# Optimization experiments

Hardware: AMD Instinct MI355X
Metric: run time of the kernel (lower is better)

The kernel has to match this reference:

```python
import jax, jax.numpy as jnp
import numpy as np

VOCAB, HIDDEN, BATCH, T = 32000, 256, 16, 256


def setup_inputs() -> dict:
    key = jax.random.key(0)
    ks = jax.random.split(key, 8)
    s_in = 1.0 / np.sqrt(HIDDEN)  # torch nn.RNN init scale (1/sqrt(hidden))
    inputs = jax.random.randint(ks[0], (BATCH, T), 0, VOCAB)
    targets = jax.random.randint(ks[1], (BATCH, T), 0, VOCAB)
    # RNN params: torch stores W_ih as (hidden, vocab); we keep the transpose
    # (vocab, hidden) so one_hot(x) @ W_ih.T == Wih[x] (an exact gather).
    Wih = jax.random.uniform(ks[2], (VOCAB, HIDDEN), minval=-s_in, maxval=s_in)
    bih = jax.random.uniform(ks[3], (HIDDEN,), minval=-s_in, maxval=s_in)
    Whh = jax.random.uniform(ks[4], (HIDDEN, HIDDEN), minval=-s_in, maxval=s_in)
    bhh = jax.random.uniform(ks[5], (HIDDEN,), minval=-s_in, maxval=s_in)
    Wfc = jax.random.uniform(ks[6], (VOCAB, HIDDEN), minval=-s_in, maxval=s_in)
    bfc = jax.random.uniform(ks[7], (VOCAB,), minval=-s_in, maxval=s_in)
    return {"inputs": inputs, "targets": targets, "Wih": Wih, "bih": bih,
            "Whh": Whh, "bhh": bhh, "Wfc": Wfc, "bfc": bfc}


def reference(inputs, targets, Wih, bih, Whh, bhh, Wfc, bfc):
    # one_hot(inputs) @ W_ih.T + b_ih  ==  Wih[inputs] + bih (exact same math)
    xproj = Wih[inputs] + bih                      # (B, T, H)
    B = inputs.shape[0]
    h0 = jnp.zeros((B, HIDDEN), dtype=Wih.dtype)

    def step(h, xt):
        h = jnp.tanh(xt + h @ Whh.T + bhh)
        return h, h

    _, hs = jax.lax.scan(step, h0, jnp.swapaxes(xproj, 0, 1))  # (T, B, H)
    hs = jnp.swapaxes(hs, 0, 1)                    # (B, T, H)
    logits = hs @ Wfc.T + bfc                      # (B, T, V)
    logp = jax.nn.log_softmax(logits, axis=-1)
    nll = -jnp.take_along_axis(logp, targets[..., None], axis=-1)
    return jnp.mean(nll)                           # scalar cross-entropy loss
```

## Files before the change

### kernel.cpp

```cpp
#include <hip/hip_runtime.h>
#include <hip/hip_bf16.h>
#include <stdint.h>

#define VOCAB 32000
#define HID   256
#define BATCH 16
#define SEQT  256
#define ROWS  (BATCH*SEQT)

typedef __attribute__((ext_vector_type(8))) short bf16x8_t;
typedef __attribute__((ext_vector_type(4))) float f32x4_t;

__device__ __forceinline__ short f2bs(float x) {
    __hip_bfloat16 h = __float2bfloat16(x);
    return *reinterpret_cast<short*>(&h);
}
__device__ __forceinline__ bf16x8_t cvt8(float4 a, float4 b) {
    union { short s[8]; bf16x8_t v; } u;
    u.s[0] = f2bs(a.x); u.s[1] = f2bs(a.y); u.s[2] = f2bs(a.z); u.s[3] = f2bs(a.w);
    u.s[4] = f2bs(b.x); u.s[5] = f2bs(b.y); u.s[6] = f2bs(b.z); u.s[7] = f2bs(b.w);
    return u.v;
}
__device__ __forceinline__ void barrier_lds() {
    asm volatile("s_waitcnt lgkmcnt(0)\n\ts_barrier" ::: "memory");
}
__device__ __forceinline__ float tanh_cf(float x) {
    float x2 = x * x;
    float nm = x * fmaf(x2, x2 + 105.f, 945.f);
    float dn = fmaf(x2, fmaf(x2, 15.f, 420.f), 945.f);
    float h = nm * __builtin_amdgcn_rcpf(dn);
    return fminf(fmaxf(h, -1.f), 1.f);
}
__device__ __forceinline__ short rne_bf16(float x) {
    uint32_t u = __float_as_uint(x);
    uint32_t r = (u + 0x7FFFu + ((u >> 16) & 1u)) >> 16;
    return (short)r;
}

__global__ __launch_bounds__(256) void xproj_kernel(
    const int* __restrict__ inputs,
    const float* __restrict__ Wih,
    const float* __restrict__ bih,
    const float* __restrict__ bhh,
    const float* __restrict__ Wfc,
    float* __restrict__ xp,
    float* __restrict__ S,
    __hip_bfloat16* __restrict__ Wfcb,
    int do_cvt)
{
    int idx = blockIdx.x * 256 + threadIdx.x;
    int h  = idx & 255;
    int tb = idx >> 8;
    int b  = tb & 15;
    int t  = tb >> 4;
    int id = inputs[b * SEQT + t];
    xp[idx] = Wih[(size_t)id * HID + h] + bih[h] + bhh[h];
    if (idx < ROWS) S[idx] = 0.0f;
    if (do_cvt && idx < (VOCAB * HID / 8)) {
        const float4* p = (const float4*)(Wfc + (size_t)idx * 8);
        *(bf16x8_t*)((short*)Wfcb + (size_t)idx * 8) = cvt8(p[0], p[1]);
    }
}

__global__ __launch_bounds__(512, 1) void rnn_kernel(
    const float* __restrict__ xp,
    const float* __restrict__ Whh,
    __hip_bfloat16* __restrict__ hs)
{
    __shared__ short hbuf[2][16][264];
    const int tid = threadIdx.x;
    const int l = tid & 63, w = tid >> 6;
    const int lr = l & 15, lh = l >> 4;
    const int cm = tid >> 5;
    const int cc = (tid & 31) * 8;

    bf16x8_t bfrag[2][8];
#pragma unroll
    for (int nt = 0; nt < 2; nt++) {
        int n = w * 32 + nt * 16 + lr;
#pragma unroll
        for (int ki = 0; ki < 8; ki++) {
            const float4* p = (const float4*)(Whh + n * HID + ki * 32 + lh * 8);
            bfrag[nt][ki] = cvt8(p[0], p[1]);
        }
    }
    for (int i = tid; i < 16 * 264; i += 512) ((short*)hbuf[0])[i] = 0;
    __syncthreads();

    float xv[2][4];
#pragma unroll
    for (int nt = 0; nt < 2; nt++) {
        int n = w * 32 + nt * 16 + lr;
#pragma unroll
        for (int r = 0; r < 4; r++)
            xv[nt][r] = xp[(lh * 4 + r) * HID + n];
    }

    int cur = 0;
    for (int t = 0; t < SEQT; t++) {
        if (t > 0) {
            bf16x8_t hv = *(const bf16x8_t*)(&hbuf[cur][cm][cc]);
            *(bf16x8_t*)((short*)hs + (size_t)(t - 1) * BATCH * HID + cm * HID + cc) = hv;
        }

        bf16x8_t afr[8];
#pragma unroll
        for (int ki = 0; ki < 8; ki++)
            afr[ki] = *(const bf16x8_t*)(&hbuf[cur][lr][ki * 32 + lh * 8]);

        f32x4_t a0a = {0,0,0,0}, a0b = {0,0,0,0}, a1a = {0,0,0,0}, a1b = {0,0,0,0};
#pragma unroll
        for (int ki = 0; ki < 4; ki++) {
            a0a = __builtin_amdgcn_mfma_f32_16x16x32_bf16(afr[ki],     bfrag[0][ki],     a0a, 0, 0, 0);
            a0b = __builtin_amdgcn_mfma_f32_16x16x32_bf16(afr[ki + 4], bfrag[0][ki + 4], a0b, 0, 0, 0);
            a1a = __builtin_amdgcn_mfma_f32_16x16x32_bf16(afr[ki],     bfrag[1][ki],     a1a, 0, 0, 0);
            a1b = __builtin_amdgcn_mfma_f32_16x16x32_bf16(afr[ki + 4], bfrag[1][ki + 4], a1b, 0, 0, 0);
        }

        float xn[2][4] = {{0,0,0,0},{0,0,0,0}};
        if (t + 1 < SEQT) {
            const float* xbase = xp + (size_t)(t + 1) * BATCH * HID;
#pragma unroll
            for (int nt = 0; nt < 2; nt++) {
                int n = w * 32 + nt * 16 + lr;
#pragma unroll
                for (int r = 0; r < 4; r++)
                    xn[nt][r] = xbase[(lh * 4 + r) * HID + n];
            }
        }

#pragma unroll
        for (int nt = 0; nt < 2; nt++) {
            int n = w * 32 + nt * 16 + lr;
#pragma unroll
            for (int r = 0; r < 4; r++) {
                float v = (nt ? (a1a[r] + a1b[r]) : (a0a[r] + a0b[r])) + xv[nt][r];
                hbuf[cur ^ 1][lh * 4 + r][n] = rne_bf16(tanh_cf(v));
            }
        }
#pragma unroll
        for (int nt = 0; nt < 2; nt++)
#pragma unroll
            for (int r = 0; r < 4; r++) xv[nt][r] = xn[nt][r];
        cur ^= 1;
        barrier_lds();
    }
    bf16x8_t hv = *(const bf16x8_t*)(&hbuf[cur][cm][cc]);
    *(bf16x8_t*)((short*)hs + (size_t)(SEQT - 1) * BATCH * HID + cm * HID + cc) = hv;
}

template <bool BF16B>
__global__ __launch_bounds__(256) void fc_kernel(
    const __hip_bfloat16* __restrict__ hs,
    const void* __restrict__ WfcP,
    const float* __restrict__ bfc,
    const int* __restrict__ targets,
    float* __restrict__ S,
    float* __restrict__ TL)
{
    __shared__ short As[2][4 * 128 * 8];
    __shared__ short Bs[2][4 * 128 * 8];
    __shared__ int tgt[128];

    const int bid = blockIdx.x;
    const int xcd = bid & 7;
    const int j   = bid >> 3;
    const int m_id = j & 31;
    const int n_id = (j >> 5) * 8 + xcd;
    if (n_id >= VOCAB / 128) return;
    const int m0 = m_id * 128, n0 = n_id * 128;

    const int tid = threadIdx.x;
    const int l = tid & 63, w = tid >> 6;
    const int lr = l & 15, lh = l >> 4;
    const int wm = (w >> 1) * 64, wn = (w & 1) * 64;
    const int row = tid & 127, sub = tid >> 7;

    if (tid < 128) {
        int r = m0 + tid;
        tgt[tid] = targets[((r & 15) << 8) | (r >> 4)];
    }

    f32x4_t acc[4][4];
    const f32x4_t z = {0.f, 0.f, 0.f, 0.f};
#pragma unroll
    for (int i = 0; i < 4; i++)
#pragma unroll
        for (int jj = 0; jj < 4; jj++) acc[i][jj] = z;

    const __hip_bfloat16* gA = hs + (size_t)(m0 + row) * HID + sub * 8;
    const __hip_bfloat16* gBb = (const __hip_bfloat16*)WfcP + (size_t)(n0 + row) * HID + sub * 8;
    const float*          gBf = (const float*)WfcP + (size_t)(n0 + row) * HID + sub * 8;

    bf16x8_t rA0, rA1, rB0, rB1;
    float4 rf0a, rf0b, rf1a, rf1b;

    {
        rA0 = *(const bf16x8_t*)(gA);
        rA1 = *(const bf16x8_t*)(gA + 16);
        *(bf16x8_t*)&As[0][(sub * 128 + row) * 8] = rA0;
        *(bf16x8_t*)&As[0][((sub + 2) * 128 + row) * 8] = rA1;
        if (BF16B) {
            rB0 = *(const bf16x8_t*)(gBb);
            rB1 = *(const bf16x8_t*)(gBb + 16);
            *(bf16x8_t*)&Bs[0][(sub * 128 + row) * 8] = rB0;
            *(bf16x8_t*)&Bs[0][((sub + 2) * 128 + row) * 8] = rB1;
        } else {
            const float4* p0 = (const float4*)(gBf);
            const float4* p1 = (const float4*)(gBf + 16);
            *(bf16x8_t*)&Bs[0][(sub * 128 + row) * 8] = cvt8(p0[0], p0[1]);
            *(bf16x8_t*)&Bs[0][((sub + 2) * 128 + row) * 8] = cvt8(p1[0], p1[1]);
        }
    }
    {
        rA0 = *(const bf16x8_t*)(gA + 32);
        rA1 = *(const bf16x8_t*)(gA + 48);
        if (BF16B) {
            rB0 = *(const bf16x8_t*)(gBb + 32);
            rB1 = *(const bf16x8_t*)(gBb + 48);
        } else {
            rf0a = ((const float4*)(gBf + 32))[0]; rf0b = ((const float4*)(gBf + 32))[1];
            rf1a = ((const float4*)(gBf + 48))[0]; rf1b = ((const float4*)(gBf + 48))[1];
        }
    }
    __syncthreads();

    for (int s = 0; s < 8; s++) {
        const int buf = s & 1;
        bf16x8_t a[4], b[4];
#pragma unroll
        for (int mt = 0; mt < 4; mt++)
            a[mt] = *(const bf16x8_t*)&As[buf][(lh * 128 + wm + mt * 16 + lr) * 8];
#pragma unroll
        for (int nt = 0; nt < 4; nt++)
            b[nt] = *(const bf16x8_t*)&Bs[buf][(lh * 128 + wn + nt * 16 + lr) * 8];

        if (s + 1 < 8) {
            *(bf16x8_t*)&As[buf ^ 1][(sub * 128 + row) * 8] = rA0;
            *(bf16x8_t*)&As[buf ^ 1][((sub + 2) * 128 + row) * 8] = rA1;
            if (BF16B) {
                *(bf16x8_t*)&Bs[buf ^ 1][(sub * 128 + row) * 8] = rB0;
                *(bf16x8_t*)&Bs[buf ^ 1][((sub + 2) * 128 + row) * 8] = rB1;
            } else {
                *(bf16x8_t*)&Bs[buf ^ 1][(sub * 128 + row) * 8] = cvt8(rf0a, rf0b);
                *(bf16x8_t*)&Bs[buf ^ 1][((sub + 2) * 128 + row) * 8] = cvt8(rf1a, rf1b);
            }
        }
        if (s + 2 < 8) {
            int k0 = (s + 2) * 32;
            rA0 = *(const bf16x8_t*)(gA + k0);
            rA1 = *(const bf16x8_t*)(gA + k0 + 16);
            if (BF16B) {
                rB0 = *(const bf16x8_t*)(gBb + k0);
                rB1 = *(const bf16x8_t*)(gBb + k0 + 16);
            } else {
                rf0a = ((const float4*)(gBf + k0))[0];      rf0b = ((const float4*)(gBf + k0))[1];
                rf1a = ((const float4*)(gBf + k0 + 16))[0]; rf1b = ((const float4*)(gBf + k0 + 16))[1];
            }
        }
#pragma unroll
        for (int mt = 0; mt < 4; mt++)
#pragma unroll
            for (int nt = 0; nt < 4; nt++)
                acc[mt][nt] = __builtin_amdgcn_mfma_f32_16x16x32_bf16(a[mt], b[nt], acc[mt][nt], 0, 0, 0);
        barrier_lds();
    }

    int tg[16];
#pragma unroll
    for (int i = 0; i < 16; i++)
        tg[i] = tgt[wm + (i >> 2) * 16 + lh * 4 + (i & 3)];

    float rsum[16];
#pragma unroll
    for (int i = 0; i < 16; i++) rsum[i] = 0.f;
#pragma unroll
    for (int nt = 0; nt < 4; nt++) {
        int n = n0 + wn + nt * 16 + lr;
        float bias = bfc[n];
#pragma unroll
        for (int mt = 0; mt < 4; mt++)
#pragma unroll
            for (int r = 0; r < 4; r++) {
                float v = acc[mt][nt][r] + bias;
                rsum[mt * 4 + r] += __expf(v);
                if (tg[mt * 4 + r] == n)
                    TL[m0 + wm + mt * 16 + lh * 4 + r] = v;
            }
    }
#pragma unroll
    for (int m = 1; m < 16; m <<= 1)
#pragma unroll
        for (int i = 0; i < 16; i++) rsum[i] += __shfl_xor(rsum[i], m, 64);
    if (lr == 0) {
#pragma unroll
        for (int i = 0; i < 16; i++) {
            int r = m0 + wm + (i >> 2) * 16 + lh * 4 + (i & 3);
            atomicAdd(&S[r], rsum[i]);
        }
    }
}

__global__ __launch_bounds__(256) void loss_kernel(
    const float* __restrict__ S,
    const float* __restrict__ TL,
    float* __restrict__ out)
{
    int tid = threadIdx.x;
    float p = 0.f;
    for (int i = tid; i < ROWS; i += 256) p += __logf(S[i]) - TL[i];
#pragma unroll
    for (int m = 1; m < 64; m <<= 1) p += __shfl_xor(p, m, 64);
    __shared__ float red[4];
    if ((tid & 63) == 0) red[tid >> 6] = p;
    __syncthreads();
    if (tid == 0)
        out[0] = (red[0] + red[1] + red[2] + red[3]) / (float)ROWS;
}

extern "C" void kernel_launch(void* const* d_in, const int* in_sizes, int n_in,
                              void* d_out, int out_size, void* d_ws, size_t ws_size,
                              hipStream_t stream)
{
    (void)in_sizes; (void)n_in; (void)out_size;
    const int*   inputs  = (const int*)d_in[0];
    const int*   targets = (const int*)d_in[1];
    const float* Wih = (const float*)d_in[2];
    const float* bih = (const float*)d_in[3];
    const float* Whh = (const float*)d_in[4];
    const float* bhh = (const float*)d_in[5];
    const float* Wfc = (const float*)d_in[6];
    const float* bfc = (const float*)d_in[7];

    float* S  = (float*)d_ws;
    float* TL = S + ROWS;
    float* xp = TL + ROWS;
    __hip_bfloat16* hs = (__hip_bfloat16*)(xp + (size_t)SEQT * BATCH * HID);
    __hip_bfloat16* Wfcb = hs + (size_t)ROWS * HID;

    const size_t need = (size_t)(2 * ROWS) * 4 + (size_t)ROWS * HID * 4
                      + (size_t)ROWS * HID * 2 + (size_t)VOCAB * HID * 2;
    const int use_bf16b = (ws_size >= need) ? 1 : 0;

    xproj_kernel<<<(SEQT * BATCH * HID) / 256, 256, 0, stream>>>(
        inputs, Wih, bih, bhh, Wfc, xp, S, Wfcb, use_bf16b);
    rnn_kernel<<<1, 512, 0, stream>>>(xp, Whh, hs);
    if (use_bf16b)
        fc_kernel<true><<<8192, 256, 0, stream>>>(hs, (const void*)Wfcb, bfc, targets, S, TL);
    else
        fc_kernel<false><<<8192, 256, 0, stream>>>(hs, (const void*)Wfc, bfc, targets, S, TL);
    loss_kernel<<<1, 256, 0, stream>>>(S, TL, (float*)d_out);
}
```

Baseline: 451.1 us.

## Fuse RNN recurrence with FC/softmax tiles via atomic-flag producer-consumer overlap

Merges the single-block RNN kernel and the FC/log-sum-exp kernel into one launch. The first block to arrive runs the recurrence and publishes progress every 8 timesteps through a global atomic counter. The remaining blocks take 256x128 output tiles and spin-wait until the hidden-state rows they need exist. This lets the large vocabulary GEMM overlap the serial recurrence instead of waiting for it to finish. It also transposes the xproj layout so each lane reads a float4, seeds the MFMA accumulators with the input projection, and enlarges the M tile to 256 with 512 threads. The cost is a deadlock risk if the recurrence block is not resident, plus spin-wait overhead and a different tile shape.

```diff
diff --git a/kernel.cpp b/kernel.cpp
--- a/kernel.cpp
+++ b/kernel.cpp
@@ -7,6 +7,9 @@
 #define BATCH 16
 #define SEQT  256
 #define ROWS  (BATCH*SEQT)
+#define NPAN  (VOCAB/128)
+#define MTILES (ROWS/256)
+#define NTILES (MTILES*NPAN)
 
 typedef __attribute__((ext_vector_type(8))) short bf16x8_t;
 typedef __attribute__((ext_vector_type(4))) float f32x4_t;
@@ -45,218 +48,203 @@
     const float* __restrict__ Wfc,
     float* __restrict__ xp,
     float* __restrict__ S,
+    unsigned* __restrict__ ctrl,
     __hip_bfloat16* __restrict__ Wfcb,
     int do_cvt)
 {
-    int idx = blockIdx.x * 256 + threadIdx.x;
-    int h  = idx & 255;
-    int tb = idx >> 8;
-    int b  = tb & 15;
-    int t  = tb >> 4;
-    int id = inputs[b * SEQT + t];
-    xp[idx] = Wih[(size_t)id * HID + h] + bih[h] + bhh[h];
-    if (idx < ROWS) S[idx] = 0.0f;
+    const int tid = threadIdx.x, blk = blockIdx.x;
+    const int t = blk >> 4, hb = (blk & 15) << 4;
+    const int b = tid & 15, h = hb + (tid >> 4);
+    const int id = inputs[b * SEQT + t];
+    xp[(t * HID + h) * BATCH + b] = Wih[(size_t)id * HID + h] + bih[h] + bhh[h];
+    const int idx = blk * 256 + tid;
+    if (idx < ROWS) S[idx] = 0.f;
+    if (idx < 2) ctrl[idx] = 0u;
     if (do_cvt && idx < (VOCAB * HID / 8)) {
         const float4* p = (const float4*)(Wfc + (size_t)idx * 8);
         *(bf16x8_t*)((short*)Wfcb + (size_t)idx * 8) = cvt8(p[0], p[1]);
     }
 }
 
-__global__ __launch_bounds__(512, 1) void rnn_kernel(
+template <bool BF16B>
+__global__ __launch_bounds__(512) void fused_kernel(
     const float* __restrict__ xp,
     const float* __restrict__ Whh,
-    __hip_bfloat16* __restrict__ hs)
-{
-    __shared__ short hbuf[2][16][264];
-    const int tid = threadIdx.x;
-    const int l = tid & 63, w = tid >> 6;
-    const int lr = l & 15, lh = l >> 4;
-    const int cm = tid >> 5;
-    const int cc = (tid & 31) * 8;
-
-    bf16x8_t bfrag[2][8];
-#pragma unroll
-    for (int nt = 0; nt < 2; nt++) {
-        int n = w * 32 + nt * 16 + lr;
-#pragma unroll
-        for (int ki = 0; ki < 8; ki++) {
-            const float4* p = (const float4*)(Whh + n * HID + ki * 32 + lh * 8);
-            bfrag[nt][ki] = cvt8(p[0], p[1]);
-        }
-    }
-    for (int i = tid; i < 16 * 264; i += 512) ((short*)hbuf[0])[i] = 0;
-    __syncthreads();
-
-    float xv[2][4];
-#pragma unroll
-    for (int nt = 0; nt < 2; nt++) {
-        int n = w * 32 + nt * 16 + lr;
-#pragma unroll
-        for (int r = 0; r < 4; r++)
-            xv[nt][r] = xp[(lh * 4 + r) * HID + n];
-    }
-
-    int cur = 0;
-    for (int t = 0; t < SEQT; t++) {
-        if (t > 0) {
-            bf16x8_t hv = *(const bf16x8_t*)(&hbuf[cur][cm][cc]);
-            *(bf16x8_t*)((short*)hs + (size_t)(t - 1) * BATCH * HID + cm * HID + cc) = hv;
-        }
-
-        bf16x8_t afr[8];
-#pragma unroll
-        for (int ki = 0; ki < 8; ki++)
-            afr[ki] = *(const bf16x8_t*)(&hbuf[cur][lr][ki * 32 + lh * 8]);
-
-        f32x4_t a0a = {0,0,0,0}, a0b = {0,0,0,0}, a1a = {0,0,0,0}, a1b = {0,0,0,0};
-#pragma unroll
-        for (int ki = 0; ki < 4; ki++) {
-            a0a = __builtin_amdgcn_mfma_f32_16x16x32_bf16(afr[ki],     bfrag[0][ki],     a0a, 0, 0, 0);
-            a0b = __builtin_amdgcn_mfma_f32_16x16x32_bf16(afr[ki + 4], bfrag[0][ki + 4], a0b, 0, 0, 0);
-            a1a = __builtin_amdgcn_mfma_f32_16x16x32_bf16(afr[ki],     bfrag[1][ki],     a1a, 0, 0, 0);
-            a1b = __builtin_amdgcn_mfma_f32_16x16x32_bf16(afr[ki + 4], bfrag[1][ki + 4], a1b, 0, 0, 0);
-        }
-
-        float xn[2][4] = {{0,0,0,0},{0,0,0,0}};
-        if (t + 1 < SEQT) {
-            const float* xbase = xp + (size_t)(t + 1) * BATCH * HID;
-#pragma unroll
-            for (int nt = 0; nt < 2; nt++) {
-                int n = w * 32 + nt * 16 + lr;
-#pragma unroll
-                for (int r = 0; r < 4; r++)
-                    xn[nt][r] = xbase[(lh * 4 + r) * HID + n];
-            }
-        }
-
-#pragma unroll
-        for (int nt = 0; nt < 2; nt++) {
-            int n = w * 32 + nt * 16 + lr;
-#pragma unroll
-            for (int r = 0; r < 4; r++) {
-                float v = (nt ? (a1a[r] + a1b[r]) : (a0a[r] + a0b[r])) + xv[nt][r];
-                hbuf[cur ^ 1][lh * 4 + r][n] = rne_bf16(tanh_cf(v));
-            }
-        }
-#pragma unroll
-        for (int nt = 0; nt < 2; nt++)
-#pragma unroll
-            for (int r = 0; r < 4; r++) xv[nt][r] = xn[nt][r];
-        cur ^= 1;
-        barrier_lds();
-    }
-    bf16x8_t hv = *(const bf16x8_t*)(&hbuf[cur][cm][cc]);
-    *(bf16x8_t*)((short*)hs + (size_t)(SEQT - 1) * BATCH * HID + cm * HID + cc) = hv;
-}
-
-template <bool BF16B>
-__global__ __launch_bounds__(256) void fc_kernel(
-    const __hip_bfloat16* __restrict__ hs,
+    __hip_bfloat16* __restrict__ hs,
     const void* __restrict__ WfcP,
     const float* __restrict__ bfc,
     const int* __restrict__ targets,
     float* __restrict__ S,
-    float* __restrict__ TL)
+    float* __restrict__ TL,
+    unsigned* __restrict__ ctrl)
 {
-    __shared__ short As[2][4 * 128 * 8];
+    __shared__ short As[2][4 * 256 * 8];
     __shared__ short Bs[2][4 * 128 * 8];
-    __shared__ int tgt[128];
-
-    const int bid = blockIdx.x;
-    const int xcd = bid & 7;
-    const int j   = bid >> 3;
-    const int m_id = j & 31;
-    const int n_id = (j >> 5) * 8 + xcd;
-    if (n_id >= VOCAB / 128) return;
-    const int m0 = m_id * 128, n0 = n_id * 128;
+    __shared__ short hbuf[2][16][264];
+    __shared__ int   tgt[256];
+    __shared__ unsigned role;
 
     const int tid = threadIdx.x;
+    if (tid == 0) role = atomicAdd(&ctrl[0], 1u);
+    __syncthreads();
+    const unsigned my_role = role;
+
     const int l = tid & 63, w = tid >> 6;
     const int lr = l & 15, lh = l >> 4;
-    const int wm = (w >> 1) * 64, wn = (w & 1) * 64;
-    const int row = tid & 127, sub = tid >> 7;
-
-    if (tid < 128) {
+
+    if (my_role == 0) {
+        const int cm = tid >> 5;
+        const int cc = (tid & 31) * 8;
+        const int n0_ = w * 32 + lr, n1_ = n0_ + 16;
+
+        bf16x8_t bfrag[2][8];
+#pragma unroll
+        for (int nt = 0; nt < 2; nt++) {
+            int n = nt ? n1_ : n0_;
+#pragma unroll
+            for (int ki = 0; ki < 8; ki++) {
+                const float4* p = (const float4*)(Whh + n * HID + ki * 32 + lh * 8);
+                bfrag[nt][ki] = cvt8(p[0], p[1]);
+            }
+        }
+        for (int i = tid; i < 16 * 264; i += 512) ((short*)hbuf[0])[i] = 0;
+        __syncthreads();
+
+        float4 xv0 = *(const float4*)(xp + (size_t)n0_ * BATCH + lh * 4);
+        float4 xv1 = *(const float4*)(xp + (size_t)n1_ * BATCH + lh * 4);
+
+        int cur = 0;
+        for (int t = 0; t < SEQT; t++) {
+            if (t > 0) {
+                bf16x8_t hv = *(const bf16x8_t*)(&hbuf[cur][cm][cc]);
+                *(bf16x8_t*)((short*)hs + (size_t)(t - 1) * BATCH * HID + cm * HID + cc) = hv;
+                if ((t & 7) == 0) {
+                    asm volatile("s_waitcnt vmcnt(0)" ::: "memory");
+                    __syncthreads();
+                    if (tid == 0)
+                        __hip_atomic_store(&ctrl[1], (unsigned)t, __ATOMIC_RELEASE,
+                                           __HIP_MEMORY_SCOPE_AGENT);
+                }
+            }
+
+            bf16x8_t afr[8];
+#pragma unroll
+            for (int ki = 0; ki < 8; ki++)
+                afr[ki] = *(const bf16x8_t*)(&hbuf[cur][lr][ki * 32 + lh * 8]);
+
+            f32x4_t a0a = {xv0.x, xv0.y, xv0.z, xv0.w}, a0b = {0, 0, 0, 0};
+            f32x4_t a1a = {xv1.x, xv1.y, xv1.z, xv1.w}, a1b = {0, 0, 0, 0};
+#pragma unroll
+            for (int ki = 0; ki < 4; ki++) {
+                a0a = __builtin_amdgcn_mfma_f32_16x16x32_bf16(afr[ki],     bfrag[0][ki],     a0a, 0, 0, 0);
+                a0b = __builtin_amdgcn_mfma_f32_16x16x32_bf16(afr[ki + 4], bfrag[0][ki + 4], a0b, 0, 0, 0);
+                a1a = __builtin_amdgcn_mfma_f32_16x16x32_bf16(afr[ki],     bfrag[1][ki],     a1a, 0, 0, 0);
+                a1b = __builtin_amdgcn_mfma_f32_16x16x32_bf16(afr[ki + 4], bfrag[1][ki + 4], a1b, 0, 0, 0);
+            }
+
+            float4 xn0 = {0,0,0,0}, xn1 = {0,0,0,0};
+            if (t + 1 < SEQT) {
+                const float* xb = xp + (size_t)(t + 1) * HID * BATCH + lh * 4;
+                xn0 = *(const float4*)(xb + (size_t)n0_ * BATCH);
+                xn1 = *(const float4*)(xb + (size_t)n1_ * BATCH);
+            }
+
+#pragma unroll
+            for (int r = 0; r < 4; r++) {
+                hbuf[cur ^ 1][lh * 4 + r][n0_] = rne_bf16(tanh_cf(a0a[r] + a0b[r]));
+                hbuf[cur ^ 1][lh * 4 + r][n1_] = rne_bf16(tanh_cf(a1a[r] + a1b[r]));
+            }
+            xv0 = xn0; xv1 = xn1;
+            cur ^= 1;
+            barrier_lds();
+        }
+        {
+            bf16x8_t hv = *(const bf16x8_t*)(&hbuf[cur][cm][cc]);
+            *(bf16x8_t*)((short*)hs + (size_t)(SEQT - 1) * BATCH * HID + cm * HID + cc) = hv;
+            asm volatile("s_waitcnt vmcnt(0)" ::: "memory");
+            __syncthreads();
+            if (tid == 0)
+                __hip_atomic_store(&ctrl[1], (unsigned)SEQT, __ATOMIC_RELEASE,
+                                   __HIP_MEMORY_SCOPE_AGENT);
+        }
+        return;
+    }
+
+    const unsigned tile = my_role - 1;
+    if (tile >= NTILES) return;
+    const int mt_ = tile / NPAN, nt_ = tile % NPAN;
+    const int m0 = mt_ * 256, n0g = nt_ * 128;
+
+    if (tid < 256) {
         int r = m0 + tid;
         tgt[tid] = targets[((r & 15) << 8) | (r >> 4)];
     }
+    if (tid == 0) {
+        const unsigned need = (unsigned)((mt_ + 1) * 16);
+        while (atomicAdd(&ctrl[1], 0u) < need)
+            __builtin_amdgcn_s_sleep(32);
+        (void)__hip_atomic_load(&ctrl[1], __ATOMIC_ACQUIRE, __HIP_MEMORY_SCOPE_AGENT);
+    }
+    __syncthreads();
+
+    const int wm = (w >> 1) * 64, wn = (w & 1) * 64;
+    const int arow = tid & 255, asub = tid >> 8;
+    const int brow = tid & 127, bsub = tid >> 7;
+
+    const __hip_bfloat16* gA = hs + (size_t)(m0 + arow) * HID + asub * 8;
+    const __hip_bfloat16* gBb = (const __hip_bfloat16*)WfcP + (size_t)(n0g + brow) * HID + bsub * 8;
+    const float*          gBf = (const float*)WfcP + (size_t)(n0g + brow) * HID + bsub * 8;
 
     f32x4_t acc[4][4];
     const f32x4_t z = {0.f, 0.f, 0.f, 0.f};
 #pragma unroll
     for (int i = 0; i < 4; i++)
 #pragma unroll
-        for (int jj = 0; jj < 4; jj++) acc[i][jj] = z;
-
-    const __hip_bfloat16* gA = hs + (size_t)(m0 + row) * HID + sub * 8;
-    const __hip_bfloat16* gBb = (const __hip_bfloat16*)WfcP + (size_t)(n0 + row) * HID + sub * 8;
-    const float*          gBf = (const float*)WfcP + (size_t)(n0 + row) * HID + sub * 8;
-
-    bf16x8_t rA0, rA1, rB0, rB1;
-    float4 rf0a, rf0b, rf1a, rf1b;
-
-    {
-        rA0 = *(const bf16x8_t*)(gA);
-        rA1 = *(const bf16x8_t*)(gA + 16);
-        *(bf16x8_t*)&As[0][(sub * 128 + row) * 8] = rA0;
-        *(bf16x8_t*)&As[0][((sub + 2) * 128 + row) * 8] = rA1;
-        if (BF16B) {
-            rB0 = *(const bf16x8_t*)(gBb);
-            rB1 = *(const bf16x8_t*)(gBb + 16);
-            *(bf16x8_t*)&Bs[0][(sub * 128 + row) * 8] = rB0;
-            *(bf16x8_t*)&Bs[0][((sub + 2) * 128 + row) * 8] = rB1;
-        } else {
-            const float4* p0 = (const float4*)(gBf);
-            const float4* p1 = (const float4*)(gBf + 16);
-            *(bf16x8_t*)&Bs[0][(sub * 128 + row) * 8] = cvt8(p0[0], p0[1]);
-            *(bf16x8_t*)&Bs[0][((sub + 2) * 128 + row) * 8] = cvt8(p1[0], p1[1]);
-        }
-    }
-    {
-        rA0 = *(const bf16x8_t*)(gA + 32);
-        rA1 = *(const bf16x8_t*)(gA + 48);
-        if (BF16B) {
-            rB0 = *(const bf16x8_t*)(gBb + 32);
-            rB1 = *(const bf16x8_t*)(gBb + 48);
-        } else {
-            rf0a = ((const float4*)(gBf + 32))[0]; rf0b = ((const float4*)(gBf + 32))[1];
-            rf1a = ((const float4*)(gBf + 48))[0]; rf1b = ((const float4*)(gBf + 48))[1];
-        }
-    }
+        for (int j = 0; j < 4; j++) acc[i][j] = z;
+
+    bf16x8_t pA0[2], pA1[2], pB[2];
+    float4 pF0[2], pF1[2];
+    pA0[0] = *(const bf16x8_t*)(gA);
+    pA1[0] = *(const bf16x8_t*)(gA + 16);
+    *(bf16x8_t*)&As[0][(asub * 256 + arow) * 8] = pA0[0];
+    *(bf16x8_t*)&As[0][((asub + 2) * 256 + arow) * 8] = pA1[0];
+    if (BF16B) {
+        pB[0] = *(const bf16x8_t*)(gBb);
+        *(bf16x8_t*)&Bs[0][(bsub * 128 + brow) * 8] = pB[0];
+    } else {
+        pF0[0] = ((const float4*)gBf)[0]; pF1[0] = ((const float4*)gBf)[1];
+        *(bf16x8_t*)&Bs[0][(bsub * 128 + brow) * 8] = cvt8(pF0[0], pF1[0]);
+    }
+    pA0[1] = *(const bf16x8_t*)(gA + 32);
+    pA1[1] = *(const bf16x8_t*)(gA + 48);
+    if (BF16B) pB[1] = *(const bf16x8_t*)(gBb + 32);
+    else { pF0[1] = ((const float4*)(gBf + 32))[0]; pF1[1] = ((const float4*)(gBf + 32))[1]; }
     __syncthreads();
 
+#pragma unroll
     for (int s = 0; s < 8; s++) {
         const int buf = s & 1;
         bf16x8_t a[4], b[4];
 #pragma unroll
         for (int mt = 0; mt < 4; mt++)
-            a[mt] = *(const bf16x8_t*)&As[buf][(lh * 128 + wm + mt * 16 + lr) * 8];
+            a[mt] = *(const bf16x8_t*)&As[buf][(lh * 256 + wm + mt * 16 + lr) * 8];
 #pragma unroll
         for (int nt = 0; nt < 4; nt++)
             b[nt] = *(const bf16x8_t*)&Bs[buf][(lh * 128 + wn + nt * 16 + lr) * 8];
 
         if (s + 1 < 8) {
-            *(bf16x8_t*)&As[buf ^ 1][(sub * 128 + row) * 8] = rA0;
-            *(bf16x8_t*)&As[buf ^ 1][((sub + 2) * 128 + row) * 8] = rA1;
-            if (BF16B) {
-                *(bf16x8_t*)&Bs[buf ^ 1][(sub * 128 + row) * 8] = rB0;
-                *(bf16x8_t*)&Bs[buf ^ 1][((sub + 2) * 128 + row) * 8] = rB1;
-            } else {
-                *(bf16x8_t*)&Bs[buf ^ 1][(sub * 128 + row) * 8] = cvt8(rf0a, rf0b);
-                *(bf16x8_t*)&Bs[buf ^ 1][((sub + 2) * 128 + row) * 8] = cvt8(rf1a, rf1b);
-            }
+            const int sl = (s + 1) & 1;
+            *(bf16x8_t*)&As[buf ^ 1][(asub * 256 + arow) * 8] = pA0[sl];
+            *(bf16x8_t*)&As[buf ^ 1][((asub + 2) * 256 + arow) * 8] = pA1[sl];
+            if (BF16B) *(bf16x8_t*)&Bs[buf ^ 1][(bsub * 128 + brow) * 8] = pB[sl];
+            else       *(bf16x8_t*)&Bs[buf ^ 1][(bsub * 128 + brow) * 8] = cvt8(pF0[sl], pF1[sl]);
         }
         if (s + 2 < 8) {
-            int k0 = (s + 2) * 32;
-            rA0 = *(const bf16x8_t*)(gA + k0);
-            rA1 = *(const bf16x8_t*)(gA + k0 + 16);
-            if (BF16B) {
-                rB0 = *(const bf16x8_t*)(gBb + k0);
-                rB1 = *(const bf16x8_t*)(gBb + k0 + 16);
-            } else {
-                rf0a = ((const float4*)(gBf + k0))[0];      rf0b = ((const float4*)(gBf + k0))[1];
-                rf1a = ((const float4*)(gBf + k0 + 16))[0]; rf1b = ((const float4*)(gBf + k0 + 16))[1];
-            }
+            const int k0 = (s + 2) * 32, sl = s & 1;
+            pA0[sl] = *(const bf16x8_t*)(gA + k0);
+            pA1[sl] = *(const bf16x8_t*)(gA + k0 + 16);
+            if (BF16B) pB[sl] = *(const bf16x8_t*)(gBb + k0);
+            else { pF0[sl] = ((const float4*)(gBf + k0))[0]; pF1[sl] = ((const float4*)(gBf + k0))[1]; }
         }
 #pragma unroll
         for (int mt = 0; mt < 4; mt++)
@@ -276,7 +264,7 @@
     for (int i = 0; i < 16; i++) rsum[i] = 0.f;
 #pragma unroll
     for (int nt = 0; nt < 4; nt++) {
-        int n = n0 + wn + nt * 16 + lr;
+        int n = n0g + wn + nt * 16 + lr;
         float bias = bfc[n];
 #pragma unroll
         for (int mt = 0; mt < 4; mt++)
@@ -332,22 +320,24 @@
     const float* Wfc = (const float*)d_in[6];
     const float* bfc = (const float*)d_in[7];
 
-    float* S  = (float*)d_ws;
-    float* TL = S + ROWS;
-    float* xp = TL + ROWS;
-    __hip_bfloat16* hs = (__hip_bfloat16*)(xp + (size_t)SEQT * BATCH * HID);
+    float*    S    = (float*)d_ws;
+    float*    TL   = S + ROWS;
+    unsigned* ctrl = (unsigned*)(TL + ROWS);
+    float*    xp   = (float*)(ctrl + 64);
+    __hip_bfloat16* hs = (__hip_bfloat16*)(xp + (size_t)SEQT * HID * BATCH);
     __hip_bfloat16* Wfcb = hs + (size_t)ROWS * HID;
 
-    const size_t need = (size_t)(2 * ROWS) * 4 + (size_t)ROWS * HID * 4
+    const size_t need = (size_t)(2 * ROWS) * 4 + 256 + (size_t)SEQT * HID * BATCH * 4
                       + (size_t)ROWS * HID * 2 + (size_t)VOCAB * HID * 2;
     const int use_bf16b = (ws_size >= need) ? 1 : 0;
 
-    xproj_kernel<<<(SEQT * BATCH * HID) / 256, 256, 0, stream>>>(
-        inputs, Wih, bih, bhh, Wfc, xp, S, Wfcb, use_bf16b);
-    rnn_kernel<<<1, 512, 0, stream>>>(xp, Whh, hs);
+    xproj_kernel<<<SEQT * 16, 256, 0, stream>>>(
+        inputs, Wih, bih, bhh, Wfc, xp, S, ctrl, Wfcb, use_bf16b);
     if (use_bf16b)
-        fc_kernel<true><<<8192, 256, 0, stream>>>(hs, (const void*)Wfcb, bfc, targets, S, TL);
+        fused_kernel<true><<<NTILES + 1, 512, 0, stream>>>(
+            xp, Whh, hs, (const void*)Wfcb, bfc, targets, S, TL, ctrl);
     else
-        fc_kernel<false><<<8192, 256, 0, stream>>>(hs, (const void*)Wfc, bfc, targets, S, TL);
+        fused_kernel<false><<<NTILES + 1, 512, 0, stream>>>(
+            xp, Whh, hs, (const void*)Wfc, bfc, targets, S, TL, ctrl);
     loss_kernel<<<1, 256, 0, stream>>>(S, TL, (float*)d_out);
 }
```

Result: slower. 803.5 us (+78.1%).
